# Kernel tuning notes

Hardware: AMD Instinct MI355X
Metric: run time of the kernel (lower is better)

## Reference

```python
import jax, jax.numpy as jnp
import numpy as np

NBINS = 10001  # hardcoded in the torch module (10000*sigmoid in [0,10000])


def setup_inputs() -> dict:
    key = jax.random.key(0)
    k1, k2 = jax.random.split(key)
    N = 33554432  # 2**25 samples
    preds = jax.random.normal(k1, (N,), dtype=jnp.float32)
    targets = jax.random.randint(k2, (N,), 0, 2).astype(jnp.float32)
    return {"preds": preds, "targets": targets}


def reference(preds, targets):
    # y_pred = int(10000 * sigmoid(preds)); truncation == floor since value >= 0
    y_pred = (10000.0 * jax.nn.sigmoid(preds)).reshape(-1).astype(jnp.int32)
    y_true = targets.reshape(-1)
    is_pos = (y_true >= 0.5).astype(preds.dtype)
    # scatter-add histogram split by label (single pass, atomic-add style)
    tpi = jnp.zeros((NBINS,), dtype=preds.dtype).at[y_pred].add(is_pos)
    fpi = jnp.zeros((NBINS,), dtype=preds.dtype).at[y_pred].add(1.0 - is_pos)
    # KS statistic: max |CDF_pos - CDF_neg|
    tp_cum = jnp.cumsum(tpi)
    fp_cum = jnp.cumsum(fpi)
    tp_curve = tp_cum / tp_cum[-1]
    fp_curve = fp_cum / fp_cum[-1]
    return jnp.max(jnp.abs(tp_curve - fp_curve))
```

## Files before the change

kernel.cpp:

```cpp
#include <hip/hip_runtime.h>

#define NBINS 10001
#define WORDS 5056
#define HIST_BLOCKS 1024
#define HIST_THREADS 512
#define PCHUNK 128
#define RCHUNKS (HIST_BLOCKS / PCHUNK)

typedef unsigned int u32;
typedef unsigned long long u64;
typedef float f4 __attribute__((ext_vector_type(4)));

__device__ __forceinline__ f4 ntload(const f4* p) {
    return __builtin_nontemporal_load(p);
}

__device__ __forceinline__ int ks_bin(float x) {
    float e = __expf(-x);
    float s = __builtin_amdgcn_rcpf(1.0f + e);
    int b = (int)(10000.0f * s);
    b = b < 0 ? 0 : b;
    return b > 10000 ? 10000 : b;
}

__device__ __forceinline__ void ks_acc4(u32* lh, f4 p, f4 t) {
#pragma unroll
    for (int k = 0; k < 4; ++k) {
        int b = ks_bin(p[k]);
        u32 add = ((t[k] >= 0.5f) ? 256u : 1u) << ((b & 1) << 4);
        atomicAdd(&lh[b >> 1], add);
    }
}

__global__ __launch_bounds__(HIST_THREADS) void ks_hist(
        const float* __restrict__ preds, const float* __restrict__ tgts,
        u64* __restrict__ ghist, u32* __restrict__ partials,
        int use_partials, int n) {
    __shared__ u32 lh[WORDS];
    for (int i = threadIdx.x; i < WORDS; i += HIST_THREADS) lh[i] = 0u;
    __syncthreads();

    const int n4 = n >> 2;
    const f4* p4 = (const f4*)preds;
    const f4* t4 = (const f4*)tgts;
    const int tid = blockIdx.x * HIST_THREADS + threadIdx.x;
    const int stride = gridDim.x * HIST_THREADS;

    const int q = n4 / stride;
    const int r = n4 - q * stride;
    const int cnt = q + (tid < r ? 1 : 0);

    f4 pA, tA, pB, tB;
    if (cnt > 0) { pA = p4[tid]; tA = ntload(t4 + tid); }
    if (cnt > 1) { pB = p4[tid + stride]; tB = ntload(t4 + tid + stride); }
    int idx = tid + stride;
    for (int k = 2; k < cnt; ++k) {
        idx += stride;
        f4 pC = p4[idx];
        f4 tC = ntload(t4 + idx);
        ks_acc4(lh, pA, tA);
        pA = pB; tA = tB;
        pB = pC; tB = tC;
    }
    if (cnt > 1) {
        ks_acc4(lh, pA, tA);
        ks_acc4(lh, pB, tB);
    } else if (cnt == 1) {
        ks_acc4(lh, pA, tA);
    }

    if (blockIdx.x == 0) {
        int base = n4 << 2;
        int rem = n - base;
        if ((int)threadIdx.x < rem) {
            int j = base + threadIdx.x;
            int b = ks_bin(preds[j]);
            u32 add = ((tgts[j] >= 0.5f) ? 256u : 1u) << ((b & 1) << 4);
            atomicAdd(&lh[b >> 1], add);
        }
    }
    __syncthreads();

    if (use_partials) {
        u32* mypart = partials + (size_t)blockIdx.x * WORDS;
        for (int j = threadIdx.x; j < WORDS; j += HIST_THREADS)
            mypart[j] = lh[j];
    } else {
        for (int b = threadIdx.x; b < NBINS; b += HIST_THREADS) {
            u32 w = lh[b >> 1];
            u32 h = (w >> ((b & 1) << 4)) & 0xFFFFu;
            if (h) {
                u64 a = ((u64)(h >> 8) << 32) | (u64)(h & 0xFFu);
                atomicAdd(&ghist[b], a);
            }
        }
    }
}

__global__ __launch_bounds__(256) void ks_reduce(const u32* __restrict__ partials,
                                                 u64* __restrict__ ghist) {
    int bin = blockIdx.x * 256 + threadIdx.x;
    if (bin >= NBINS) return;
    const int word = bin >> 1;
    const int sh = (bin & 1) << 4;
    const u32* base = partials + (size_t)blockIdx.y * PCHUNK * WORDS;
    u32 tp = 0, fp = 0;
#pragma unroll 4
    for (int k = 0; k < PCHUNK; ++k) {
        u32 h = (base[(size_t)k * WORDS + word] >> sh) & 0xFFFFu;
        tp += h >> 8;
        fp += h & 0xFFu;
    }
    atomicAdd(&ghist[bin], ((u64)tp << 32) | (u64)fp);
}

__global__ __launch_bounds__(1024) void ks_scan(const u64* __restrict__ ghist,
                                                float* __restrict__ out) {
    __shared__ long long stp[1024];
    __shared__ long long sfp[1024];
    __shared__ double smx[1024];

    const int t = threadIdx.x;
    const int CH = 10;
    const int lo = t * CH;

    u64 loc[CH];
    long long tps = 0, fps = 0;
#pragma unroll
    for (int k = 0; k < CH; ++k) {
        int i = lo + k;
        u64 v = (i < NBINS) ? ghist[i] : 0ull;
        loc[k] = v;
        tps += (long long)(v >> 32);
        fps += (long long)(v & 0xFFFFFFFFull);
    }
    stp[t] = tps;
    sfp[t] = fps;
    __syncthreads();

    for (int off = 1; off < 1024; off <<= 1) {
        long long a = stp[t], b = sfp[t];
        long long c = 0, d = 0;
        if (t >= off) { c = stp[t - off]; d = sfp[t - off]; }
        __syncthreads();
        stp[t] = a + c;
        sfp[t] = b + d;
        __syncthreads();
    }

    const long long TP = stp[1023];
    const long long FP = sfp[1023];
    const long long etp = stp[t] - tps;
    const long long efp = sfp[t] - fps;

    const double invTP = 1.0 / (double)(TP > 0 ? TP : 1);
    const double invFP = 1.0 / (double)(FP > 0 ? FP : 1);

    double m = 0.0;
    long long tc = etp, fc = efp;
#pragma unroll
    for (int k = 0; k < CH; ++k) {
        u64 v = loc[k];
        tc += (long long)(v >> 32);
        fc += (long long)(v & 0xFFFFFFFFull);
        double d = fabs((double)tc * invTP - (double)fc * invFP);
        m = (d > m) ? d : m;
    }

    smx[t] = m;
    __syncthreads();
    for (int off = 512; off > 0; off >>= 1) {
        if (t < off) smx[t] = smx[t] > smx[t + off] ? smx[t] : smx[t + off];
        __syncthreads();
    }
    if (t == 0) out[0] = (float)smx[0];
}

extern "C" void kernel_launch(void* const* d_in, const int* in_sizes, int n_in,
                              void* d_out, int out_size, void* d_ws, size_t ws_size,
                              hipStream_t stream) {
    const float* preds = (const float*)d_in[0];
    const float* tgts  = (const float*)d_in[1];
    const int n = in_sizes[0];

    const size_t part_off = 131072;
    const size_t need = part_off + (size_t)HIST_BLOCKS * WORDS * sizeof(u32);
    u64* ghist = (u64*)d_ws;
    u32* partials = (u32*)((char*)d_ws + part_off);
    const int use_partials = (ws_size >= need) ? 1 : 0;

    hipMemsetAsync(d_ws, 0, NBINS * sizeof(u64), stream);

    ks_hist<<<HIST_BLOCKS, HIST_THREADS, 0, stream>>>(preds, tgts, ghist,
                                                      partials, use_partials, n);
    if (use_partials) {
        dim3 rg((NBINS + 255) / 256, RCHUNKS);
        ks_reduce<<<rg, 256, 0, stream>>>(partials, ghist);
    }
    ks_scan<<<1, 1024, 0, stream>>>(ghist, (float*)d_out);
}
```

Baseline: 72.25 us.

## Hand-pipeline histogram loads with inline asm and explicit vmcnt waits

Replaces the compiler-scheduled double-buffered loop with a four-deep software pipeline. Global loads are issued through inline asm and gated by explicit s_waitcnt vmcnt counters, and the LDS atomic adds go out as raw ds_add_u32 instructions after the bin addresses are computed. The aim is to keep more loads in flight and stop the compiler from inserting conservative waits between the shared-memory atomics and the global loads. This relies on fragile asm register constraints and on exact vmcnt accounting, and it keeps a fallback path for sizes that don't divide evenly.

```diff
diff --git a/kernel.cpp b/kernel.cpp
--- a/kernel.cpp
+++ b/kernel.cpp
@@ -23,13 +23,44 @@
     return b > 10000 ? 10000 : b;
 }
 
-__device__ __forceinline__ void ks_acc4(u32* lh, f4 p, f4 t) {
+__device__ __forceinline__ void ks_bins4(u32* lh, f4 p, f4 t, u32* Ad, u32* Av) {
 #pragma unroll
     for (int k = 0; k < 4; ++k) {
         int b = ks_bin(p[k]);
-        u32 add = ((t[k] >= 0.5f) ? 256u : 1u) << ((b & 1) << 4);
-        atomicAdd(&lh[b >> 1], add);
-    }
+        Ad[k] = (u32)(size_t)(&lh[b >> 1]);
+        Av[k] = ((t[k] >= 0.5f) ? 256u : 1u) << ((b & 1) << 4);
+    }
+}
+
+__device__ __forceinline__ void ks_fire4(const u32* Ad, const u32* Av) {
+    asm volatile(
+        "ds_add_u32 %0, %4\n\t"
+        "ds_add_u32 %1, %5\n\t"
+        "ds_add_u32 %2, %6\n\t"
+        "ds_add_u32 %3, %7"
+        :: "v"(Ad[0]), "v"(Ad[1]), "v"(Ad[2]), "v"(Ad[3]),
+           "v"(Av[0]), "v"(Av[1]), "v"(Av[2]), "v"(Av[3]));
+}
+
+__device__ __forceinline__ void load2_asm(u64 pa, u64 ta, f4& p, f4& t) {
+    asm volatile(
+        "global_load_dwordx4 %0, %2, off\n\t"
+        "global_load_dwordx4 %1, %3, off nt"
+        : "=&v"(p), "=&v"(t)
+        : "v"(pa), "v"(ta));
+}
+
+__device__ __forceinline__ void wait_vm6(f4& p, f4& t) {
+    asm volatile("s_waitcnt vmcnt(6)" : "+v"(p), "+v"(t));
+}
+__device__ __forceinline__ void wait_vm4(f4& p, f4& t) {
+    asm volatile("s_waitcnt vmcnt(4)" : "+v"(p), "+v"(t));
+}
+__device__ __forceinline__ void wait_vm2(f4& p, f4& t) {
+    asm volatile("s_waitcnt vmcnt(2)" : "+v"(p), "+v"(t));
+}
+__device__ __forceinline__ void wait_vm0(f4& p, f4& t) {
+    asm volatile("s_waitcnt vmcnt(0)" : "+v"(p), "+v"(t));
 }
 
 __global__ __launch_bounds__(HIST_THREADS) void ks_hist(
@@ -48,25 +79,90 @@
 
     const int q = n4 / stride;
     const int r = n4 - q * stride;
-    const int cnt = q + (tid < r ? 1 : 0);
-
-    f4 pA, tA, pB, tB;
-    if (cnt > 0) { pA = p4[tid]; tA = ntload(t4 + tid); }
-    if (cnt > 1) { pB = p4[tid + stride]; tB = ntload(t4 + tid + stride); }
-    int idx = tid + stride;
-    for (int k = 2; k < cnt; ++k) {
-        idx += stride;
-        f4 pC = p4[idx];
-        f4 tC = ntload(t4 + idx);
-        ks_acc4(lh, pA, tA);
-        pA = pB; tA = tB;
-        pB = pC; tB = tC;
-    }
-    if (cnt > 1) {
-        ks_acc4(lh, pA, tA);
-        ks_acc4(lh, pB, tB);
-    } else if (cnt == 1) {
-        ks_acc4(lh, pA, tA);
+
+    if (q >= 8 && (q & 3) == 0) {
+        u64 pbase = (u64)(size_t)(p4 + tid);
+        u64 tbase = (u64)(size_t)(t4 + tid);
+        const u64 stepB = (u64)stride * 16u;
+
+        f4 p0, t0, p1, t1, p2, t2, p3, t3;
+        u32 Ad[4], Av[4];
+
+        load2_asm(pbase,             tbase,             p0, t0);
+        load2_asm(pbase + stepB,     tbase + stepB,     p1, t1);
+        load2_asm(pbase + 2 * stepB, tbase + 2 * stepB, p2, t2);
+        load2_asm(pbase + 3 * stepB, tbase + 3 * stepB, p3, t3);
+        wait_vm6(p0, t0);
+        ks_bins4(lh, p0, t0, Ad, Av);
+
+#define KS_STEADY(GIDX, PL, TL, PU, TU)                                     \
+        ks_fire4(Ad, Av);                                                   \
+        load2_asm(pbase + (u64)((GIDX) + 3) * stepB,                        \
+                  tbase + (u64)((GIDX) + 3) * stepB, PL, TL);               \
+        wait_vm6(PU, TU);                                                   \
+        ks_bins4(lh, PU, TU, Ad, Av);
+
+        for (int g = 1; g + 3 <= q - 4; g += 4) {
+            KS_STEADY(g,     p0, t0, p1, t1)
+            KS_STEADY(g + 1, p1, t1, p2, t2)
+            KS_STEADY(g + 2, p2, t2, p3, t3)
+            KS_STEADY(g + 3, p3, t3, p0, t0)
+        }
+#undef KS_STEADY
+        ks_fire4(Ad, Av);
+        wait_vm4(p1, t1);
+        ks_bins4(lh, p1, t1, Ad, Av);
+        ks_fire4(Ad, Av);
+        wait_vm2(p2, t2);
+        ks_bins4(lh, p2, t2, Ad, Av);
+        ks_fire4(Ad, Av);
+        wait_vm0(p3, t3);
+        ks_bins4(lh, p3, t3, Ad, Av);
+        ks_fire4(Ad, Av);
+
+        if (tid < r) {
+            f4 p = p4[tid + q * stride];
+            f4 t = ntload(t4 + tid + q * stride);
+#pragma unroll
+            for (int k = 0; k < 4; ++k) {
+                int b = ks_bin(p[k]);
+                u32 add = ((t[k] >= 0.5f) ? 256u : 1u) << ((b & 1) << 4);
+                atomicAdd(&lh[b >> 1], add);
+            }
+        }
+    } else {
+        const int cnt = q + (tid < r ? 1 : 0);
+        f4 pA, tA, pB, tB;
+        if (cnt > 0) { pA = p4[tid]; tA = ntload(t4 + tid); }
+        if (cnt > 1) { pB = p4[tid + stride]; tB = ntload(t4 + tid + stride); }
+        int idx = tid + stride;
+        for (int k = 2; k < cnt; ++k) {
+            idx += stride;
+            f4 pC = p4[idx];
+            f4 tC = ntload(t4 + idx);
+#pragma unroll
+            for (int e = 0; e < 4; ++e) {
+                int b = ks_bin(pA[e]);
+                u32 add = ((tA[e] >= 0.5f) ? 256u : 1u) << ((b & 1) << 4);
+                atomicAdd(&lh[b >> 1], add);
+            }
+            pA = pB; tA = tB;
+            pB = pC; tB = tC;
+        }
+        for (int s = 0; s < 2; ++s) {
+            if (cnt > s + 0 && (s == 0 ? cnt > 0 : cnt > 1)) {
+                f4 p = (s == 0) ? pA : pB;
+                f4 t = (s == 0) ? tA : tB;
+                if ((s == 1 && cnt > 1) || (s == 0 && cnt > 0)) {
+#pragma unroll
+                    for (int e = 0; e < 4; ++e) {
+                        int b = ks_bin(p[e]);
+                        u32 add = ((t[e] >= 0.5f) ? 256u : 1u) << ((b & 1) << 4);
+                        atomicAdd(&lh[b >> 1], add);
+                    }
+                }
+            }
+        }
     }
 
     if (blockIdx.x == 0) {
@@ -79,6 +175,8 @@
             atomicAdd(&lh[b >> 1], add);
         }
     }
+
+    asm volatile("s_waitcnt vmcnt(0) lgkmcnt(0)" ::: "memory");
     __syncthreads();
 
     if (use_partials) {
```

Result: no change. 72.16 us (-0.1%).
